# Kernel tuning notes

Hardware: AMD Instinct MI355X
Metric: run time of the kernel (lower is better)

## Reference

```python
import jax, jax.numpy as jnp
import numpy as np

B, LAT, NF, IMG, N_CALLS = 8, 512, 64, 128, 4
N_LAYERS = int(np.ceil(np.log2(IMG) - np.log2(16))) + 1  # 4 resolutions: 16,32,64,128
CF = 3  # SinSobel perception factor: identity + sobel_x + sobel_y
FIN, FH, FOUT = NF * CF, NF, NF * 2  # gated => 2*n_filter out of dyna block
P_SIZES = [FH * FIN, FH, FOUT * FH, FOUT, FOUT * FIN, FOUT]
P_OFFS = np.cumsum([0] + P_SIZES)
P_TOT = int(P_OFFS[-1])

_g1 = np.exp(-0.5 * np.array([-1.0, 0.0, 1.0]) ** 2)
_gk = np.outer(_g1, _g1); _gk = _gk / _gk.sum()
GAUSS_K = jnp.asarray(_gk, jnp.float32)
SOBEL_X = jnp.asarray(np.array([[-1, 0, 1], [-2, 0, 2], [-1, 0, 1]], np.float32) / 8.0)
SOBEL_Y = SOBEL_X.T


def _dwconv3(x, k):
    # depthwise 3x3 conv, 'same' padding; x: [B,C,H,W], k: [3,3]
    C = x.shape[1]
    kern = jnp.broadcast_to(k[None, None], (C, 1, 3, 3)).astype(x.dtype)
    return jax.lax.conv_general_dilated(
        x, kern, (1, 1), ((1, 1), (1, 1)),
        dimension_numbers=('NCHW', 'OIHW', 'NCHW'), feature_group_count=C)


def sin_sobel(x):
    # perception: [x, sobel_x(x), sobel_y(x)] -> 3*C channels
    return jnp.concatenate([x, _dwconv3(x, SOBEL_X), _dwconv3(x, SOBEL_Y)], axis=1)


def inst_norm(x, eps=1e-5):
    m = x.mean((2, 3), keepdims=True)
    v = x.var((2, 3), keepdims=True)
    return (x - m) * jax.lax.rsqrt(v + eps)


def up2_blur(x, gk):
    b, c, h, w = x.shape
    x = jax.image.resize(x, (b, c, 2 * h, 2 * w), 'bilinear')  # align_corners=False
    return _dwconv3(x, gk)


def dyna_block(x, lat, hyper_w, hyper_b):
    # hypernetwork generates per-sample 1x1-conv residual block weights
    p = lat @ hyper_w + hyper_b  # [B, P_TOT]
    w1 = p[:, P_OFFS[0]:P_OFFS[1]].reshape(-1, FH, FIN)
    b1 = p[:, P_OFFS[1]:P_OFFS[2]]
    w2 = p[:, P_OFFS[2]:P_OFFS[3]].reshape(-1, FOUT, FH)
    b2 = p[:, P_OFFS[3]:P_OFFS[4]]
    ws = p[:, P_OFFS[4]:P_OFFS[5]].reshape(-1, FOUT, FIN)
    bs = p[:, P_OFFS[5]:P_OFFS[6]]
    h = jax.nn.relu(jnp.einsum('bihw,boi->bohw', x, w1) + b1[:, :, None, None])
    y = jnp.einsum('bihw,boi->bohw', h, w2) + b2[:, :, None, None]
    s = jnp.einsum('bihw,boi->bohw', x, ws) + bs[:, :, None, None]
    return s + y


def setup_inputs() -> dict:
    key = jax.random.key(0)
    ks = jax.random.split(key, 8)
    return dict(
        lat=jax.random.normal(ks[0], (B, LAT), jnp.float32),
        ca_noise=jax.random.normal(ks[1], (B, NF, 16, 16), jnp.float32),
        seed=jax.random.normal(ks[2], (1, NF, 1, 1), jnp.float32),  # spatially constant seed
        leak_factor=jnp.asarray(0.1, jnp.float32),
        hyper_w=jax.random.normal(ks[3], (LAT, P_TOT), jnp.float32) * 0.02,
        hyper_b=jnp.zeros((P_TOT,), jnp.float32),
        res1_w=jax.random.normal(ks[4], (NF, NF), jnp.float32) / np.sqrt(NF).astype(np.float32),
        res1_b=jnp.zeros((NF,), jnp.float32),
        res2_w=jax.random.normal(ks[5], (NF, NF), jnp.float32) / np.sqrt(NF).astype(np.float32),
        res2_b=jnp.zeros((NF,), jnp.float32),
        outc_w=jax.random.normal(ks[6], (3, NF), jnp.float32) / np.sqrt(NF).astype(np.float32),
        outc_b=jnp.zeros((3,), jnp.float32),
    )


def reference(lat, ca_noise, seed, leak_factor, hyper_w, hyper_b,
              res1_w, res1_b, res2_w, res2_b, outc_w, outc_b):
    # seed init branch: constant seed -> instance_norm -> 0, plus blurred ca_noise
    out = inst_norm(jnp.broadcast_to(seed, (B, NF, 16, 16)))
    out = out + _dwconv3(ca_noise, GAUSS_K)  # in_ds (resize 16->16 is identity)
    lf = jnp.clip(leak_factor, 0.001, 1000.0)
    for c in range(N_LAYERS * N_CALLS):
        z = sin_sobel(out)
        z = inst_norm(z)
        z = dyna_block(z, lat, hyper_w, hyper_b)
        z, g = jnp.split(z, 2, axis=1)  # gated
        z = z * jax.nn.sigmoid(g)
        out = out + lf * z
        if c < N_LAYERS * N_CALLS - 1 and c % N_CALLS == N_CALLS - 1:
            out = up2_blur(out, GAUSS_K)
    # out_conv: resize to IMG is identity here; 1x1 residual block + 1x1 conv
    h = jax.nn.relu(jnp.einsum('bihw,oi->bohw', out, res1_w) + res1_b[None, :, None, None])
    r = jnp.einsum('bihw,oi->bohw', h, res2_w) + res2_b[None, :, None, None]
    y = jnp.einsum('bihw,oi->bohw', out + r, outc_w) + outc_b[None, :, None, None]
    out_raw = y
    return jnp.clip(y, -1.0, 1.0), out_raw
```

## Files before the change

### kernel.cpp

```cpp
#include <hip/hip_runtime.h>
#include <math.h>

#define B 8
#define LATD 512
#define PT 45376
#define FIN 192
#define FH 64
#define OW1 0
#define OB1 12288
#define OW2 12352
#define OB2 20544
#define OWS 20672
#define OBS 45248
#define KC 16

__device__ __forceinline__ float gk_at(int ky, int kx){
  const float a = 0.60653065971263342f;
  const float inv = 1.0f / ((1.0f + 2.0f*a) * (1.0f + 2.0f*a));
  float wy = (ky==1) ? 1.0f : a;
  float wx = (kx==1) ? 1.0f : a;
  return wy * wx * inv;
}

__global__ void k_hyper(const float* __restrict__ lat, const float* __restrict__ hw,
                        const float* __restrict__ hb, float* __restrict__ p){
  __shared__ float slat[B*LATD];
  for (int idx = threadIdx.x; idx < B*LATD; idx += 256) slat[idx] = lat[idx];
  __syncthreads();
  int j = blockIdx.x*256 + threadIdx.x;
  if (j >= PT) return;
  float acc[B];
#pragma unroll
  for (int b=0;b<B;++b) acc[b]=0.f;
  for (int k=0;k<LATD;++k){
    float w = hw[(size_t)k*PT + j];
#pragma unroll
    for (int b=0;b<B;++b) acc[b] = fmaf(slat[b*LATD+k], w, acc[b]);
  }
  float bias = hb[j];
#pragma unroll
  for (int b=0;b<B;++b) p[(size_t)b*PT + j] = acc[b] + bias;
}

__global__ void k_init(const float* __restrict__ noise, float* __restrict__ out){
  int bc = blockIdx.x;
  int t = threadIdx.x;
  int y = t >> 4, x = t & 15;
  const float* src = noise + (size_t)bc*256;
  float acc = 0.f;
#pragma unroll
  for (int ky=0;ky<3;++ky){
    int yy = y+ky-1; if (yy < 0 || yy > 15) continue;
#pragma unroll
    for (int kx=0;kx<3;++kx){
      int xx = x+kx-1; if (xx < 0 || xx > 15) continue;
      acc = fmaf(gk_at(ky,kx), src[yy*16+xx], acc);
    }
  }
  out[(size_t)bc*256 + t] = acc;
}

__global__ void __launch_bounds__(256) k_sobstat(const float* __restrict__ out, float* __restrict__ sob,
                    float* __restrict__ stats, int H, int lgH, int HW){
  int flat = blockIdx.x; int b = flat & 7, c = flat >> 3;
  int t = threadIdx.x;
  const float* src = out + ((size_t)(b*64+c))*(size_t)HW;
  float* dxp = sob + ((size_t)(b*128 + c))*(size_t)HW;
  float* dyp = sob + ((size_t)(b*128 + 64 + c))*(size_t)HW;
  float s0=0.f,q0=0.f,sx=0.f,qx=0.f,sy=0.f,qy=0.f;
  for (int px = t*4; px < HW; px += 1024){
    int y = px >> lgH, x = px & (H-1);
    float rm[6], rc[6], rp[6];
    float4 v = *(const float4*)(src + px);
    rc[1]=v.x; rc[2]=v.y; rc[3]=v.z; rc[4]=v.w;
    rc[0] = (x>0)     ? src[px-1] : 0.f;
    rc[5] = (x+4 < H) ? src[px+4] : 0.f;
    s0 += v.x+v.y+v.z+v.w;
    q0 += v.x*v.x+v.y*v.y+v.z*v.z+v.w*v.w;
    if (y > 0){
      const float* r = src + px - H;
      float4 u = *(const float4*)r;
      rm[1]=u.x; rm[2]=u.y; rm[3]=u.z; rm[4]=u.w;
      rm[0] = (x>0)     ? r[-1] : 0.f;
      rm[5] = (x+4 < H) ? r[4]  : 0.f;
    } else { rm[0]=rm[1]=rm[2]=rm[3]=rm[4]=rm[5]=0.f; }
    if (y+1 < H){
      const float* r = src + px + H;
      float4 u = *(const float4*)r;
      rp[1]=u.x; rp[2]=u.y; rp[3]=u.z; rp[4]=u.w;
      rp[0] = (x>0)     ? r[-1] : 0.f;
      rp[5] = (x+4 < H) ? r[4]  : 0.f;
    } else { rp[0]=rp[1]=rp[2]=rp[3]=rp[4]=rp[5]=0.f; }
    float dxv[4], dyv[4];
#pragma unroll
    for (int j=0;j<4;++j){
      dxv[j] = ((rm[j+2]-rm[j]) + 2.f*(rc[j+2]-rc[j]) + (rp[j+2]-rp[j])) * 0.125f;
      dyv[j] = ((rp[j] + 2.f*rp[j+1] + rp[j+2]) - (rm[j] + 2.f*rm[j+1] + rm[j+2])) * 0.125f;
      sx += dxv[j]; qx = fmaf(dxv[j],dxv[j],qx);
      sy += dyv[j]; qy = fmaf(dyv[j],dyv[j],qy);
    }
    float4 o1; o1.x=dxv[0]; o1.y=dxv[1]; o1.z=dxv[2]; o1.w=dxv[3];
    float4 o2; o2.x=dyv[0]; o2.y=dyv[1]; o2.z=dyv[2]; o2.w=dyv[3];
    *(float4*)(dxp + px) = o1;
    *(float4*)(dyp + px) = o2;
  }
  float vals[6] = {s0,q0,sx,qx,sy,qy};
  __shared__ float rbuf[6][4];
  int lane = t & 63, wid = t >> 6;
#pragma unroll
  for (int i=0;i<6;++i){
    float v = vals[i];
#pragma unroll
    for (int off=32; off; off>>=1) v += __shfl_down(v, off, 64);
    if (lane==0) rbuf[i][wid] = v;
  }
  __syncthreads();
  if (t < 3){
    float s = rbuf[t*2][0]+rbuf[t*2][1]+rbuf[t*2][2]+rbuf[t*2][3];
    float q = rbuf[t*2+1][0]+rbuf[t*2+1][1]+rbuf[t*2+1][2]+rbuf[t*2+1][3];
    float inv = 1.0f/(float)HW;
    float m = s*inv;
    float var = fmaxf(q*inv - m*m, 0.f);
    float r = 1.0f/sqrtf(var + 1e-5f);
    int ch = b*192 + c + t*64;
    stats[ch*2]   = -m*r;
    stats[ch*2+1] = r;
  }
}

__device__ __forceinline__ float4 ldx(const float* __restrict__ out, const float* __restrict__ sob,
                                      const float* __restrict__ stats,
                                      int b, int i, int off, int HW){
  const float* src = (i < 64) ? out + ((size_t)(b*64+i))*(size_t)HW
                              : sob + ((size_t)(b*128+(i-64)))*(size_t)HW;
  float4 v = *(const float4*)(src + off);
  float c = stats[(b*192+i)*2], r = stats[(b*192+i)*2+1];
  v.x = fmaf(v.x, r, c); v.y = fmaf(v.y, r, c);
  v.z = fmaf(v.z, r, c); v.w = fmaf(v.w, r, c);
  return v;
}

template<int PPT>
__global__ void __launch_bounds__(256, 3) k_dyna(float* __restrict__ out, const float* __restrict__ sob,
                       const float* __restrict__ stats, const float* __restrict__ p,
                       const float* __restrict__ lfp, int HW){
  constexpr int G     = PPT/4;
  constexpr int TPXT  = 16*PPT;
  constexpr int XST   = TPXT + 4;
  constexpr int XHALF = KC*XST;
  constexpr int W1OFF = 2*XHALF;
  constexpr int W1HALF= KC*68;
  constexpr int WEND  = W1OFF + 2*W1HALF;
  constexpr int HSZ   = 64*XST;
  constexpr int ASZ   = (WEND > HSZ) ? WEND : HSZ;
  __shared__ float bufA[ASZ];
  __shared__ float bufB[2*KC*132];

  int flat = (int)(blockIdx.y*gridDim.x + blockIdx.x);
  int b   = flat & 7;
  int px0 = (flat >> 3) * TPXT;
  int tx = threadIdx.x, ty = threadIdx.y;
  int tid = ty*16 + tx;
  const float* pw = p + (size_t)b*PT;

  float az[4][PPT], ag[4][PPT], ah[4][PPT];
#pragma unroll
  for (int k=0;k<4;++k)
#pragma unroll
    for (int j=0;j<PPT;++j){ az[k][j]=0.f; ag[k][j]=0.f; ah[k][j]=0.f; }

  const int wo0 = tid>>2, wk = tid&3, wo1 = 64 + wo0;

  float4 vx[G], vz0, vz1, v10;

  auto loadX = [&](int ci){
#pragma unroll
    for (int g=0; g<G; ++g){
      int idx = g*256 + tid;
      vx[g] = ldx(out,sob,stats,b, ci*KC + idx/(4*PPT), px0 + (idx&(4*PPT-1))*4, HW);
    }
  };
  auto loadW1z = [&](int ci){
    vz0 = *(const float4*)(pw + OWS + wo0*FIN + ci*KC + wk*4);
    vz1 = *(const float4*)(pw + OWS + wo1*FIN + ci*KC + wk*4);
    v10 = *(const float4*)(pw + OW1 + wo0*FIN + ci*KC + wk*4);
  };
  auto loadW2 = [&](int ci){
    vz0 = *(const float4*)(pw + OW2 + wo0*FH + ci*KC + wk*4);
    vz1 = *(const float4*)(pw + OW2 + wo1*FH + ci*KC + wk*4);
  };
  auto writeX = [&](int bf){
#pragma unroll
    for (int g=0; g<G; ++g){
      int idx = g*256 + tid;
      *(float4*)(&bufA[bf*XHALF + (idx/(4*PPT))*XST + (idx&(4*PPT-1))*4]) = vx[g];
    }
  };
  auto writeWz = [&](int bf){
    float* WZ = &bufB[bf*(KC*132)];
    WZ[(wk*4+0)*132+wo0]=vz0.x; WZ[(wk*4+1)*132+wo0]=vz0.y; WZ[(wk*4+2)*132+wo0]=vz0.z; WZ[(wk*4+3)*132+wo0]=vz0.w;
    WZ[(wk*4+0)*132+wo1]=vz1.x; WZ[(wk*4+1)*132+wo1]=vz1.y; WZ[(wk*4+2)*132+wo1]=vz1.z; WZ[(wk*4+3)*132+wo1]=vz1.w;
  };
  auto writeW1 = [&](int bf){
    float* W1 = &bufA[W1OFF + bf*W1HALF];
    W1[(wk*4+0)*68+wo0]=v10.x; W1[(wk*4+1)*68+wo0]=v10.y; W1[(wk*4+2)*68+wo0]=v10.z; W1[(wk*4+3)*68+wo0]=v10.w;
  };
  auto computeA = [&](int bf){
#pragma unroll 4
    for (int kk=0; kk<KC; ++kk){
      float xv[PPT];
#pragma unroll
      for (int g=0; g<G; ++g){
        float4 xa = *(const float4*)(&bufA[bf*XHALF + kk*XST + (tx+g*16)*4]);
        xv[g*4+0]=xa.x; xv[g*4+1]=xa.y; xv[g*4+2]=xa.z; xv[g*4+3]=xa.w;
      }
      float4 wz4 = *(const float4*)(&bufB[bf*(KC*132) + kk*132 + ty*4]);
      float4 wg4 = *(const float4*)(&bufB[bf*(KC*132) + kk*132 + 64 + ty*4]);
      float4 w14 = *(const float4*)(&bufA[W1OFF + bf*W1HALF + kk*68 + ty*4]);
      float wzv[4]={wz4.x,wz4.y,wz4.z,wz4.w};
      float wgv[4]={wg4.x,wg4.y,wg4.z,wg4.w};
      float w1v[4]={w14.x,w14.y,w14.z,w14.w};
#pragma unroll
      for (int k=0;k<4;++k)
#pragma unroll
        for (int j=0;j<PPT;++j){
          az[k][j] = fmaf(wzv[k], xv[j], az[k][j]);
          ag[k][j] = fmaf(wgv[k], xv[j], ag[k][j]);
          ah[k][j] = fmaf(w1v[k], xv[j], ah[k][j]);
        }
    }
  };

  loadX(0); loadW1z(0);
  writeX(0); writeWz(0); writeW1(0);
  loadX(1); loadW1z(1);
  __syncthreads();
  for (int ci=0; ci<12; ++ci){
    int cur = ci & 1;
    if (ci < 11){ writeX(cur^1); writeWz(cur^1); writeW1(cur^1); }
    if (ci < 10){ loadX(ci+2); loadW1z(ci+2); }
    else if (ci == 10){ loadW2(0); }
    computeA(cur);
    __syncthreads();
  }

#pragma unroll
  for (int k=0;k<4;++k){
    float b1 = pw[OB1 + ty*4 + k];
#pragma unroll
    for (int h=0; h<G; ++h){
      float4 r;
      r.x = fmaxf(ah[k][h*4+0]+b1, 0.f);
      r.y = fmaxf(ah[k][h*4+1]+b1, 0.f);
      r.z = fmaxf(ah[k][h*4+2]+b1, 0.f);
      r.w = fmaxf(ah[k][h*4+3]+b1, 0.f);
      *(float4*)(&bufA[(ty*4+k)*XST + (tx+h*16)*4]) = r;
    }
  }
  writeWz(0);
  loadW2(1);
  __syncthreads();

  for (int ci=0; ci<4; ++ci){
    int cur = ci & 1;
    if (ci < 3) writeWz(cur^1);
    if (ci < 2) loadW2(ci+2);
#pragma unroll 4
    for (int kk=0; kk<KC; ++kk){
      float xv[PPT];
#pragma unroll
      for (int g=0; g<G; ++g){
        float4 xa = *(const float4*)(&bufA[(ci*KC+kk)*XST + (tx+g*16)*4]);
        xv[g*4+0]=xa.x; xv[g*4+1]=xa.y; xv[g*4+2]=xa.z; xv[g*4+3]=xa.w;
      }
      float4 wz4 = *(const float4*)(&bufB[cur*(KC*132) + kk*132 + ty*4]);
      float4 wg4 = *(const float4*)(&bufB[cur*(KC*132) + kk*132 + 64 + ty*4]);
      float wzv[4]={wz4.x,wz4.y,wz4.z,wz4.w};
      float wgv[4]={wg4.x,wg4.y,wg4.z,wg4.w};
#pragma unroll
      for (int k=0;k<4;++k)
#pragma unroll
        for (int j=0;j<PPT;++j){
          az[k][j] = fmaf(wzv[k], xv[j], az[k][j]);
          ag[k][j] = fmaf(wgv[k], xv[j], ag[k][j]);
        }
    }
    __syncthreads();
  }

  float lf = fminf(fmaxf(lfp[0], 0.001f), 1000.f);
#pragma unroll
  for (int k=0;k<4;++k){
    int o = ty*4 + k;
    float bz = pw[OB2 + o]      + pw[OBS + o];
    float bg = pw[OB2 + o + 64] + pw[OBS + o + 64];
    float* op = out + ((size_t)(b*64+o))*(size_t)HW + px0;
#pragma unroll
    for (int h=0; h<G; ++h){
      float4 ov = *(const float4*)(op + (tx + h*16)*4);
      float r[4];
#pragma unroll
      for (int j=0;j<4;++j){
        float z = az[k][h*4+j] + bz;
        float g = ag[k][h*4+j] + bg;
        r[j] = lf * z / (1.f + expf(-g));
      }
      ov.x += r[0]; ov.y += r[1]; ov.z += r[2]; ov.w += r[3];
      *(float4*)(op + (tx + h*16)*4) = ov;
    }
  }
}

__global__ void k_upsample(const float* __restrict__ src, float* __restrict__ dst, int H, int lgH){
  int Hn = 2*H;
  int HWn = Hn*Hn;
  int bc = blockIdx.y;
  int o4 = (blockIdx.x*256 + threadIdx.x)*4;
  const float* s = src + (size_t)bc*(size_t)(H*H);
  int oy = o4 >> (lgH+1), ox0 = o4 & (Hn-1);
  int m = ox0 >> 1;
  int xm1 = (m-1 < 0)   ? 0   : m-1;
  int xp1 = (m+1 > H-1) ? H-1 : m+1;
  int xp2 = (m+2 > H-1) ? H-1 : m+2;
  float u[3][6];
#pragma unroll
  for (int ky=0; ky<3; ++ky){
    int yy = oy + ky - 1;
    if (yy < 0 || yy >= Hn){
#pragma unroll
      for (int j=0;j<6;++j) u[ky][j] = 0.f;
      continue;
    }
    int iy = yy >> 1, ry = yy & 1;
    int y0 = ry ? iy : iy-1;
    int y1 = ry ? iy+1 : iy;
    float wy0 = ry ? 0.75f : 0.25f;
    float wy1 = 1.f - wy0;
    y0 = y0 < 0 ? 0 : y0;
    y1 = y1 > H-1 ? H-1 : y1;
    const float* r0 = s + y0*H;
    const float* r1 = s + y1*H;
    float sv0 = wy0*r0[xm1] + wy1*r1[xm1];
    float sv1 = wy0*r0[m]   + wy1*r1[m];
    float sv2 = wy0*r0[xp1] + wy1*r1[xp1];
    float sv3 = wy0*r0[xp2] + wy1*r1[xp2];
    u[ky][0] = 0.75f*sv0 + 0.25f*sv1;
    u[ky][1] = 0.25f*sv0 + 0.75f*sv1;
    u[ky][2] = 0.75f*sv1 + 0.25f*sv2;
    u[ky][3] = 0.25f*sv1 + 0.75f*sv2;
    u[ky][4] = 0.75f*sv2 + 0.25f*sv3;
    u[ky][5] = 0.25f*sv2 + 0.75f*sv3;
    if (ox0 == 0)       u[ky][0] = 0.f;
    if (ox0 + 4 == Hn)  u[ky][5] = 0.f;
  }
  float res[4];
#pragma unroll
  for (int jo=0; jo<4; ++jo){
    float a = 0.f;
#pragma unroll
    for (int ky=0; ky<3; ++ky){
      a = fmaf(gk_at(ky,0), u[ky][jo],   a);
      a = fmaf(gk_at(ky,1), u[ky][jo+1], a);
      a = fmaf(gk_at(ky,2), u[ky][jo+2], a);
    }
    res[jo] = a;
  }
  float4 o; o.x=res[0]; o.y=res[1]; o.z=res[2]; o.w=res[3];
  *(float4*)(dst + (size_t)bc*(size_t)HWn + o4) = o;
}

__global__ void __launch_bounds__(256) k_final(const float* __restrict__ t,
    const float* __restrict__ r1w, const float* __restrict__ r1b,
    const float* __restrict__ r2w, const float* __restrict__ r2b,
    const float* __restrict__ ocw, const float* __restrict__ ocb,
    float* __restrict__ dout, int HW){
  __shared__ float Ts[64][132];
  __shared__ float Hs[64][132];
  __shared__ float Wb[64][68];
  int b = blockIdx.y;
  int tx = threadIdx.x, ty = threadIdx.y;
  int tid = ty*16 + tx;
  int px0 = blockIdx.x*128;

#pragma unroll
  for (int it=0; it<8; ++it){
    int idx = it*256 + tid;
    int ch = idx>>5, c4 = idx&31;
    *(float4*)(&Ts[ch][c4*4]) = *(const float4*)(t + ((size_t)(b*64+ch))*(size_t)HW + px0 + c4*4);
  }
#pragma unroll
  for (int it=0; it<4; ++it){
    int idx = it*256 + tid;
    int o = idx>>4, k4 = idx&15;
    float4 w = *(const float4*)(r1w + o*64 + k4*4);
    Wb[k4*4+0][o]=w.x; Wb[k4*4+1][o]=w.y; Wb[k4*4+2][o]=w.z; Wb[k4*4+3][o]=w.w;
  }
  __syncthreads();

  float acc[4][8];
#pragma unroll
  for (int k=0;k<4;++k)
#pragma unroll
    for (int j=0;j<8;++j) acc[k][j]=0.f;
#pragma unroll 4
  for (int kk=0; kk<64; ++kk){
    float4 xa = *(const float4*)(&Ts[kk][tx*4]);
    float4 xb = *(const float4*)(&Ts[kk][(tx+16)*4]);
    float4 w4 = *(const float4*)(&Wb[kk][ty*4]);
    float xv[8]={xa.x,xa.y,xa.z,xa.w,xb.x,xb.y,xb.z,xb.w};
    float wv[4]={w4.x,w4.y,w4.z,w4.w};
#pragma unroll
    for (int k=0;k<4;++k)
#pragma unroll
      for (int j=0;j<8;++j) acc[k][j] = fmaf(wv[k], xv[j], acc[k][j]);
  }
  __syncthreads();

#pragma unroll
  for (int k=0;k<4;++k){
    float bs = r1b[ty*4+k];
#pragma unroll
    for (int h=0; h<2; ++h){
      float4 r;
      r.x = fmaxf(acc[k][h*4+0]+bs, 0.f);
      r.y = fmaxf(acc[k][h*4+1]+bs, 0.f);
      r.z = fmaxf(acc[k][h*4+2]+bs, 0.f);
      r.w = fmaxf(acc[k][h*4+3]+bs, 0.f);
      *(float4*)(&Hs[ty*4+k][(tx+h*16)*4]) = r;
    }
  }
#pragma unroll
  for (int it=0; it<4; ++it){
    int idx = it*256 + tid;
    int o = idx>>4, k4 = idx&15;
    float4 w = *(const float4*)(r2w + o*64 + k4*4);
    Wb[k4*4+0][o]=w.x; Wb[k4*4+1][o]=w.y; Wb[k4*4+2][o]=w.z; Wb[k4*4+3][o]=w.w;
  }
  __syncthreads();

#pragma unroll
  for (int k=0;k<4;++k)
#pragma unroll
    for (int j=0;j<8;++j) acc[k][j]=0.f;
#pragma unroll 4
  for (int kk=0; kk<64; ++kk){
    float4 xa = *(const float4*)(&Hs[kk][tx*4]);
    float4 xb = *(const float4*)(&Hs[kk][(tx+16)*4]);
    float4 w4 = *(const float4*)(&Wb[kk][ty*4]);
    float xv[8]={xa.x,xa.y,xa.z,xa.w,xb.x,xb.y,xb.z,xb.w};
    float wv[4]={w4.x,w4.y,w4.z,w4.w};
#pragma unroll
    for (int k=0;k<4;++k)
#pragma unroll
      for (int j=0;j<8;++j) acc[k][j] = fmaf(wv[k], xv[j], acc[k][j]);
  }
#pragma unroll
  for (int k=0;k<4;++k){
    int o = ty*4 + k;
    float bs = r2b[o];
#pragma unroll
    for (int h=0; h<2; ++h){
      float4 tv = *(const float4*)(&Ts[o][(tx+h*16)*4]);
      tv.x += acc[k][h*4+0]+bs; tv.y += acc[k][h*4+1]+bs;
      tv.z += acc[k][h*4+2]+bs; tv.w += acc[k][h*4+3]+bs;
      *(float4*)(&Ts[o][(tx+h*16)*4]) = tv;
    }
  }
  __syncthreads();
  if (tid < 192){
    int c = tid>>6, kk = tid&63;
    Wb[kk][c] = ocw[c*64+kk];
  }
  __syncthreads();

  if (tid < 128){
    float a0=0.f, a1=0.f, a2=0.f;
#pragma unroll 4
    for (int kk=0; kk<64; ++kk){
      float x = Ts[kk][tid];
      a0 = fmaf(x, Wb[kk][0], a0);
      a1 = fmaf(x, Wb[kk][1], a1);
      a2 = fmaf(x, Wb[kk][2], a2);
    }
    size_t rawoff = (size_t)B*3*(size_t)HW;
    float y[3] = {a0+ocb[0], a1+ocb[1], a2+ocb[2]};
    int px = px0 + tid;
#pragma unroll
    for (int c=0;c<3;++c){
      size_t base = ((size_t)(b*3+c))*(size_t)HW + px;
      dout[base] = fminf(fmaxf(y[c],-1.f),1.f);
      dout[rawoff + base] = y[c];
    }
  }
}

extern "C" void kernel_launch(void* const* d_in, const int* in_sizes, int n_in,
                              void* d_out, int out_size, void* d_ws, size_t ws_size,
                              hipStream_t stream) {
  const float* lat = (const float*)d_in[0];
  const float* ca  = (const float*)d_in[1];
  const float* lfp = (const float*)d_in[3];
  const float* hw  = (const float*)d_in[4];
  const float* hb  = (const float*)d_in[5];
  const float* r1w = (const float*)d_in[6];
  const float* r1b = (const float*)d_in[7];
  const float* r2w = (const float*)d_in[8];
  const float* r2b = (const float*)d_in[9];
  const float* ocw = (const float*)d_in[10];
  const float* ocb = (const float*)d_in[11];
  float* dout = (float*)d_out;

  float* ws   = (float*)d_ws;
  float* p    = ws;
  float* outA = p    + (size_t)B*PT;
  float* outB = outA + (size_t)B*64*16384;
  float* sob  = outB + (size_t)B*64*16384;
  float* stats= sob  + (size_t)B*128*16384;

  k_hyper<<<dim3((PT+255)/256), dim3(256), 0, stream>>>(lat, hw, hb, p);
  k_init<<<dim3(B*64), dim3(256), 0, stream>>>(ca, outA);

  float* cur = outA;
  float* oth = outB;
  int H = 16, lgH = 4;
  for (int c = 0; c < 16; ++c){
    int HW = H*H;
    k_sobstat<<<dim3(B*64), dim3(256), 0, stream>>>(cur, sob, stats, H, lgH, HW);
    if (H >= 128)
      k_dyna<8><<<dim3(HW/128, B), dim3(16,16), 0, stream>>>(cur, sob, stats, p, lfp, HW);
    else
      k_dyna<4><<<dim3(HW/64,  B), dim3(16,16), 0, stream>>>(cur, sob, stats, p, lfp, HW);
    if (c < 15 && (c & 3) == 3){
      k_upsample<<<dim3((HW*4)/1024, B*64), dim3(256), 0, stream>>>(cur, oth, H, lgH);
      float* tmp = cur; cur = oth; oth = tmp;
      H *= 2; lgH += 1;
    }
  }
  int HW = H*H;
  k_final<<<dim3(HW/128, B), dim3(16,16), 0, stream>>>(cur, r1w, r1b, r2w, r2b, ocw, ocb, dout, HW);
}
```

Measured before the change: 1.313 ms.

## Fuse low-resolution stages into one cooperative persistent kernel with grid syncs

The first 12 CA steps (16, 32 and 64 resolution), plus the init blur and the upsamples, now run inside one cooperative kernel of 256 blocks. Grid-wide syncs separate the stages, replacing about 30 small kernel launches whose grids underfill the GPU. The sobel/stat kernel at 128 resolution now uses 1024 threads per plane instead of 256. Each grid sync has its own cost, and the persistent blocks loop over dyna tiles, so the small stages may still be latency-bound. If the cooperative launch fails, the code falls back to separate launches.

```diff
diff --git a/kernel.cpp b/kernel.cpp
--- a/kernel.cpp
+++ b/kernel.cpp
@@ -1,5 +1,8 @@
 #include <hip/hip_runtime.h>
+#include <hip/hip_cooperative_groups.h>
 #include <math.h>
+
+namespace cg = cooperative_groups;
 
 #define B 8
 #define LATD 512
@@ -60,15 +63,24 @@
   out[(size_t)bc*256 + t] = acc;
 }
 
-__global__ void __launch_bounds__(256) k_sobstat(const float* __restrict__ out, float* __restrict__ sob,
-                    float* __restrict__ stats, int H, int lgH, int HW){
-  int flat = blockIdx.x; int b = flat & 7, c = flat >> 3;
-  int t = threadIdx.x;
-  const float* src = out + ((size_t)(b*64+c))*(size_t)HW;
-  float* dxp = sob + ((size_t)(b*128 + c))*(size_t)HW;
-  float* dyp = sob + ((size_t)(b*128 + 64 + c))*(size_t)HW;
+__device__ __forceinline__ float4 ldx(const float* __restrict__ out, const float* __restrict__ sob,
+                                      const float* __restrict__ stats,
+                                      int b, int i, int off, int HW){
+  const float* src = (i < 64) ? out + ((size_t)(b*64+i))*(size_t)HW
+                              : sob + ((size_t)(b*128+(i-64)))*(size_t)HW;
+  float4 v = *(const float4*)(src + off);
+  float c = stats[(b*192+i)*2], r = stats[(b*192+i)*2+1];
+  v.x = fmaf(v.x, r, c); v.y = fmaf(v.y, r, c);
+  v.z = fmaf(v.z, r, c); v.w = fmaf(v.w, r, c);
+  return v;
+}
+
+__device__ void sobstat_body(const float* __restrict__ src, float* __restrict__ dxp,
+                             float* __restrict__ dyp, float* __restrict__ stats,
+                             float* rbufRaw, int statbase, int H, int lgH, int HW,
+                             int tid, int nthr){
   float s0=0.f,q0=0.f,sx=0.f,qx=0.f,sy=0.f,qy=0.f;
-  for (int px = t*4; px < HW; px += 1024){
+  for (int px = tid*4; px < HW; px += nthr*4){
     int y = px >> lgH, x = px & (H-1);
     float rm[6], rc[6], rp[6];
     float4 v = *(const float4*)(src + px);
@@ -105,8 +117,8 @@
     *(float4*)(dyp + px) = o2;
   }
   float vals[6] = {s0,q0,sx,qx,sy,qy};
-  __shared__ float rbuf[6][4];
-  int lane = t & 63, wid = t >> 6;
+  float (*rbuf)[16] = (float(*)[16])rbufRaw;
+  int lane = tid & 63, wid = tid >> 6;
 #pragma unroll
   for (int i=0;i<6;++i){
     float v = vals[i];
@@ -115,29 +127,291 @@
     if (lane==0) rbuf[i][wid] = v;
   }
   __syncthreads();
-  if (t < 3){
-    float s = rbuf[t*2][0]+rbuf[t*2][1]+rbuf[t*2][2]+rbuf[t*2][3];
-    float q = rbuf[t*2+1][0]+rbuf[t*2+1][1]+rbuf[t*2+1][2]+rbuf[t*2+1][3];
+  if (tid < 3){
+    int nw = nthr >> 6;
+    float s = 0.f, q = 0.f;
+    for (int i2=0;i2<nw;++i2){ s += rbuf[tid*2][i2]; q += rbuf[tid*2+1][i2]; }
     float inv = 1.0f/(float)HW;
     float m = s*inv;
     float var = fmaxf(q*inv - m*m, 0.f);
     float r = 1.0f/sqrtf(var + 1e-5f);
-    int ch = b*192 + c + t*64;
-    stats[ch*2]   = -m*r;
-    stats[ch*2+1] = r;
-  }
-}
-
-__device__ __forceinline__ float4 ldx(const float* __restrict__ out, const float* __restrict__ sob,
-                                      const float* __restrict__ stats,
-                                      int b, int i, int off, int HW){
-  const float* src = (i < 64) ? out + ((size_t)(b*64+i))*(size_t)HW
-                              : sob + ((size_t)(b*128+(i-64)))*(size_t)HW;
-  float4 v = *(const float4*)(src + off);
-  float c = stats[(b*192+i)*2], r = stats[(b*192+i)*2+1];
-  v.x = fmaf(v.x, r, c); v.y = fmaf(v.y, r, c);
-  v.z = fmaf(v.z, r, c); v.w = fmaf(v.w, r, c);
-  return v;
+    stats[(statbase + tid*64)*2]   = -m*r;
+    stats[(statbase + tid*64)*2+1] = r;
+  }
+  __syncthreads();
+}
+
+__device__ void dyna4_body(float* __restrict__ cur, const float* __restrict__ sob,
+                           const float* __restrict__ stats, const float* __restrict__ pw,
+                           float* bufA, float* bufB, int b, int px0, int HW,
+                           int tx, int ty, int tid, float lf){
+  float az[4][4], ag[4][4], ah[4][4];
+#pragma unroll
+  for (int k=0;k<4;++k)
+#pragma unroll
+    for (int j=0;j<4;++j){ az[k][j]=0.f; ag[k][j]=0.f; ah[k][j]=0.f; }
+  const int wo0 = tid>>2, wk = tid&3, wo1 = 64 + wo0;
+  float4 vx, vz0, vz1, v10;
+
+  auto loadX = [&](int ci){ vx = ldx(cur,sob,stats,b, ci*KC + ty, px0 + tx*4, HW); };
+  auto loadW1z = [&](int ci){
+    vz0 = *(const float4*)(pw + OWS + wo0*FIN + ci*KC + wk*4);
+    vz1 = *(const float4*)(pw + OWS + wo1*FIN + ci*KC + wk*4);
+    v10 = *(const float4*)(pw + OW1 + wo0*FIN + ci*KC + wk*4);
+  };
+  auto loadW2 = [&](int ci){
+    vz0 = *(const float4*)(pw + OW2 + wo0*FH + ci*KC + wk*4);
+    vz1 = *(const float4*)(pw + OW2 + wo1*FH + ci*KC + wk*4);
+  };
+  auto writeX = [&](int bf){ *(float4*)(&bufA[bf*1088 + ty*68 + tx*4]) = vx; };
+  auto writeWz = [&](int bf){
+    float* WZ = &bufB[bf*2112];
+    WZ[(wk*4+0)*132+wo0]=vz0.x; WZ[(wk*4+1)*132+wo0]=vz0.y; WZ[(wk*4+2)*132+wo0]=vz0.z; WZ[(wk*4+3)*132+wo0]=vz0.w;
+    WZ[(wk*4+0)*132+wo1]=vz1.x; WZ[(wk*4+1)*132+wo1]=vz1.y; WZ[(wk*4+2)*132+wo1]=vz1.z; WZ[(wk*4+3)*132+wo1]=vz1.w;
+  };
+  auto writeW1 = [&](int bf){
+    float* W1 = &bufA[2176 + bf*1088];
+    W1[(wk*4+0)*68+wo0]=v10.x; W1[(wk*4+1)*68+wo0]=v10.y; W1[(wk*4+2)*68+wo0]=v10.z; W1[(wk*4+3)*68+wo0]=v10.w;
+  };
+
+  loadX(0); loadW1z(0);
+  writeX(0); writeWz(0); writeW1(0);
+  loadX(1); loadW1z(1);
+  __syncthreads();
+  for (int ci=0; ci<12; ++ci){
+    int curb = ci & 1;
+    if (ci < 11){ writeX(curb^1); writeWz(curb^1); writeW1(curb^1); }
+    if (ci < 10){ loadX(ci+2); loadW1z(ci+2); }
+    else if (ci == 10){ loadW2(0); }
+#pragma unroll 4
+    for (int kk=0; kk<KC; ++kk){
+      float4 xa = *(const float4*)(&bufA[curb*1088 + kk*68 + tx*4]);
+      float4 wz4 = *(const float4*)(&bufB[curb*2112 + kk*132 + ty*4]);
+      float4 wg4 = *(const float4*)(&bufB[curb*2112 + kk*132 + 64 + ty*4]);
+      float4 w14 = *(const float4*)(&bufA[2176 + curb*1088 + kk*68 + ty*4]);
+      float xv[4]={xa.x,xa.y,xa.z,xa.w};
+      float wzv[4]={wz4.x,wz4.y,wz4.z,wz4.w};
+      float wgv[4]={wg4.x,wg4.y,wg4.z,wg4.w};
+      float w1v[4]={w14.x,w14.y,w14.z,w14.w};
+#pragma unroll
+      for (int k=0;k<4;++k)
+#pragma unroll
+        for (int j=0;j<4;++j){
+          az[k][j] = fmaf(wzv[k], xv[j], az[k][j]);
+          ag[k][j] = fmaf(wgv[k], xv[j], ag[k][j]);
+          ah[k][j] = fmaf(w1v[k], xv[j], ah[k][j]);
+        }
+    }
+    __syncthreads();
+  }
+#pragma unroll
+  for (int k=0;k<4;++k){
+    float b1 = pw[OB1 + ty*4 + k];
+    float4 r;
+    r.x = fmaxf(ah[k][0]+b1, 0.f);
+    r.y = fmaxf(ah[k][1]+b1, 0.f);
+    r.z = fmaxf(ah[k][2]+b1, 0.f);
+    r.w = fmaxf(ah[k][3]+b1, 0.f);
+    *(float4*)(&bufA[(ty*4+k)*68 + tx*4]) = r;
+  }
+  writeWz(0);
+  loadW2(1);
+  __syncthreads();
+  for (int ci=0; ci<4; ++ci){
+    int curb = ci & 1;
+    if (ci < 3) writeWz(curb^1);
+    if (ci < 2) loadW2(ci+2);
+#pragma unroll 4
+    for (int kk=0; kk<KC; ++kk){
+      float4 xa = *(const float4*)(&bufA[(ci*KC+kk)*68 + tx*4]);
+      float4 wz4 = *(const float4*)(&bufB[curb*2112 + kk*132 + ty*4]);
+      float4 wg4 = *(const float4*)(&bufB[curb*2112 + kk*132 + 64 + ty*4]);
+      float xv[4]={xa.x,xa.y,xa.z,xa.w};
+      float wzv[4]={wz4.x,wz4.y,wz4.z,wz4.w};
+      float wgv[4]={wg4.x,wg4.y,wg4.z,wg4.w};
+#pragma unroll
+      for (int k=0;k<4;++k)
+#pragma unroll
+        for (int j=0;j<4;++j){
+          az[k][j] = fmaf(wzv[k], xv[j], az[k][j]);
+          ag[k][j] = fmaf(wgv[k], xv[j], ag[k][j]);
+        }
+    }
+    __syncthreads();
+  }
+#pragma unroll
+  for (int k=0;k<4;++k){
+    int o = ty*4 + k;
+    float bz = pw[OB2 + o]      + pw[OBS + o];
+    float bg = pw[OB2 + o + 64] + pw[OBS + o + 64];
+    float* op = cur + ((size_t)(b*64+o))*(size_t)HW + px0;
+    float4 ov = *(const float4*)(op + tx*4);
+    float r[4];
+#pragma unroll
+    for (int j=0;j<4;++j){
+      float z = az[k][j] + bz;
+      float g = ag[k][j] + bg;
+      r[j] = lf * z / (1.f + expf(-g));
+    }
+    ov.x += r[0]; ov.y += r[1]; ov.z += r[2]; ov.w += r[3];
+    *(float4*)(op + tx*4) = ov;
+  }
+}
+
+__device__ void upsample_body(const float* __restrict__ s, float* __restrict__ d,
+                              int H, int lgH, int tid, int nthr){
+  int Hn = 2*H, HWn = Hn*Hn;
+  for (int o4 = tid*4; o4 < HWn; o4 += nthr*4){
+    int oy = o4 >> (lgH+1), ox0 = o4 & (Hn-1);
+    int m = ox0 >> 1;
+    int xm1 = (m-1 < 0)   ? 0   : m-1;
+    int xp1 = (m+1 > H-1) ? H-1 : m+1;
+    int xp2 = (m+2 > H-1) ? H-1 : m+2;
+    float u[3][6];
+#pragma unroll
+    for (int ky=0; ky<3; ++ky){
+      int yy = oy + ky - 1;
+      if (yy < 0 || yy >= Hn){
+#pragma unroll
+        for (int j=0;j<6;++j) u[ky][j] = 0.f;
+        continue;
+      }
+      int iy = yy >> 1, ry = yy & 1;
+      int y0 = ry ? iy : iy-1;
+      int y1 = ry ? iy+1 : iy;
+      float wy0 = ry ? 0.75f : 0.25f;
+      float wy1 = 1.f - wy0;
+      y0 = y0 < 0 ? 0 : y0;
+      y1 = y1 > H-1 ? H-1 : y1;
+      const float* r0 = s + y0*H;
+      const float* r1 = s + y1*H;
+      float sv0 = wy0*r0[xm1] + wy1*r1[xm1];
+      float sv1 = wy0*r0[m]   + wy1*r1[m];
+      float sv2 = wy0*r0[xp1] + wy1*r1[xp1];
+      float sv3 = wy0*r0[xp2] + wy1*r1[xp2];
+      u[ky][0] = 0.75f*sv0 + 0.25f*sv1;
+      u[ky][1] = 0.25f*sv0 + 0.75f*sv1;
+      u[ky][2] = 0.75f*sv1 + 0.25f*sv2;
+      u[ky][3] = 0.25f*sv1 + 0.75f*sv2;
+      u[ky][4] = 0.75f*sv2 + 0.25f*sv3;
+      u[ky][5] = 0.25f*sv2 + 0.75f*sv3;
+      if (ox0 == 0)       u[ky][0] = 0.f;
+      if (ox0 + 4 == Hn)  u[ky][5] = 0.f;
+    }
+    float res[4];
+#pragma unroll
+    for (int jo=0; jo<4; ++jo){
+      float a = 0.f;
+#pragma unroll
+      for (int ky=0; ky<3; ++ky){
+        a = fmaf(gk_at(ky,0), u[ky][jo],   a);
+        a = fmaf(gk_at(ky,1), u[ky][jo+1], a);
+        a = fmaf(gk_at(ky,2), u[ky][jo+2], a);
+      }
+      res[jo] = a;
+    }
+    float4 o; o.x=res[0]; o.y=res[1]; o.z=res[2]; o.w=res[3];
+    *(float4*)(d + o4) = o;
+  }
+}
+
+__global__ void __launch_bounds__(256, 3) k_small(float* __restrict__ outA, float* __restrict__ outB,
+    const float* __restrict__ ca, float* __restrict__ sob, float* __restrict__ stats,
+    const float* __restrict__ p, const float* __restrict__ lfp){
+  cg::grid_group grid = cg::this_grid();
+  __shared__ float bufA[4352];
+  __shared__ float bufB[4224];
+  int bid = (int)blockIdx.x;
+  int tx = threadIdx.x, ty = threadIdx.y;
+  int tid = ty*16 + tx;
+
+#pragma unroll
+  for (int it=0; it<2; ++it){
+    int bc = bid + it*256;
+    int y = tid >> 4, x = tid & 15;
+    const float* src = ca + (size_t)bc*256;
+    float acc = 0.f;
+#pragma unroll
+    for (int ky=0;ky<3;++ky){
+      int yy = y+ky-1; if (yy < 0 || yy > 15) continue;
+#pragma unroll
+      for (int kx=0;kx<3;++kx){
+        int xx = x+kx-1; if (xx < 0 || xx > 15) continue;
+        acc = fmaf(gk_at(ky,kx), src[yy*16+xx], acc);
+      }
+    }
+    outA[(size_t)bc*256 + tid] = acc;
+  }
+  grid.sync();
+
+  float* cur = outA; float* oth = outB;
+  int H = 16, lgH = 4;
+  float lf = fminf(fmaxf(lfp[0], 0.001f), 1000.f);
+
+  for (int c = 0; c < 12; ++c){
+    int HW = H*H;
+#pragma unroll
+    for (int it=0; it<2; ++it){
+      int cid = bid + it*256;
+      int b = cid & 7, ch = cid >> 3;
+      sobstat_body(cur + ((size_t)(b*64+ch))*(size_t)HW,
+                   sob + ((size_t)(b*128+ch))*(size_t)HW,
+                   sob + ((size_t)(b*128+64+ch))*(size_t)HW,
+                   stats, bufA, b*192 + ch, H, lgH, HW, tid, 256);
+    }
+    grid.sync();
+
+    int nT = (HW/64)*8;
+    for (int t = bid; t < nT; t += 256){
+      int b = t & 7;
+      int px0 = (t >> 3) * 64;
+      dyna4_body(cur, sob, stats, p + (size_t)b*PT, bufA, bufB, b, px0, HW, tx, ty, tid, lf);
+      __syncthreads();
+    }
+    grid.sync();
+
+    if ((c & 3) == 3){
+      int HWn = 4*HW;
+#pragma unroll
+      for (int it=0; it<2; ++it){
+        int plane = bid + it*256;
+        upsample_body(cur + (size_t)plane*(size_t)HW, oth + (size_t)plane*(size_t)HWn,
+                      H, lgH, tid, 256);
+      }
+      grid.sync();
+      float* tsw = cur; cur = oth; oth = tsw;
+      H *= 2; lgH += 1;
+    }
+  }
+}
+
+__global__ void __launch_bounds__(1024) k_sobstat(const float* __restrict__ out, float* __restrict__ sob,
+                    float* __restrict__ stats, int H, int lgH, int HW){
+  __shared__ float rbuf[6*16];
+  int flat = blockIdx.x; int b = flat & 7, c = flat >> 3;
+  sobstat_body(out + ((size_t)(b*64+c))*(size_t)HW,
+               sob + ((size_t)(b*128+c))*(size_t)HW,
+               sob + ((size_t)(b*128+64+c))*(size_t)HW,
+               stats, rbuf, b*192 + c, H, lgH, HW, (int)threadIdx.x, (int)blockDim.x);
+}
+
+__global__ void __launch_bounds__(256, 3) k_dyna4(float* __restrict__ out, const float* __restrict__ sob,
+                       const float* __restrict__ stats, const float* __restrict__ p,
+                       const float* __restrict__ lfp, int HW){
+  __shared__ float bufA[4352];
+  __shared__ float bufB[4224];
+  int flat = (int)(blockIdx.y*gridDim.x + blockIdx.x);
+  int b   = flat & 7;
+  int px0 = (flat >> 3) * 64;
+  float lf = fminf(fmaxf(lfp[0], 0.001f), 1000.f);
+  dyna4_body(out, sob, stats, p + (size_t)b*PT, bufA, bufB, b, px0, HW,
+             (int)threadIdx.x, (int)threadIdx.y, (int)(threadIdx.y*16+threadIdx.x), lf);
+}
+
+__global__ void k_upsample(const float* __restrict__ src, float* __restrict__ dst, int H, int lgH){
+  int bc = blockIdx.x;
+  upsample_body(src + (size_t)bc*(size_t)(H*H), dst + (size_t)bc*(size_t)(4*H*H),
+                H, lgH, (int)threadIdx.x, (int)blockDim.x);
 }
 
 template<int PPT>
@@ -170,7 +444,6 @@
     for (int j=0;j<PPT;++j){ az[k][j]=0.f; ag[k][j]=0.f; ah[k][j]=0.f; }
 
   const int wo0 = tid>>2, wk = tid&3, wo1 = 64 + wo0;
-
   float4 vx[G], vz0, vz1, v10;
 
   auto loadX = [&](int ci){
@@ -309,64 +582,6 @@
       *(float4*)(op + (tx + h*16)*4) = ov;
     }
   }
-}
-
-__global__ void k_upsample(const float* __restrict__ src, float* __restrict__ dst, int H, int lgH){
-  int Hn = 2*H;
-  int HWn = Hn*Hn;
-  int bc = blockIdx.y;
-  int o4 = (blockIdx.x*256 + threadIdx.x)*4;
-  const float* s = src + (size_t)bc*(size_t)(H*H);
-  int oy = o4 >> (lgH+1), ox0 = o4 & (Hn-1);
-  int m = ox0 >> 1;
-  int xm1 = (m-1 < 0)   ? 0   : m-1;
-  int xp1 = (m+1 > H-1) ? H-1 : m+1;
-  int xp2 = (m+2 > H-1) ? H-1 : m+2;
-  float u[3][6];
-#pragma unroll
-  for (int ky=0; ky<3; ++ky){
-    int yy = oy + ky - 1;
-    if (yy < 0 || yy >= Hn){
-#pragma unroll
-      for (int j=0;j<6;++j) u[ky][j] = 0.f;
-      continue;
-    }
-    int iy = yy >> 1, ry = yy & 1;
-    int y0 = ry ? iy : iy-1;
-    int y1 = ry ? iy+1 : iy;
-    float wy0 = ry ? 0.75f : 0.25f;
-    float wy1 = 1.f - wy0;
-    y0 = y0 < 0 ? 0 : y0;
-    y1 = y1 > H-1 ? H-1 : y1;
-    const float* r0 = s + y0*H;
-    const float* r1 = s + y1*H;
-    float sv0 = wy0*r0[xm1] + wy1*r1[xm1];
-    float sv1 = wy0*r0[m]   + wy1*r1[m];
-    float sv2 = wy0*r0[xp1] + wy1*r1[xp1];
-    float sv3 = wy0*r0[xp2] + wy1*r1[xp2];
-    u[ky][0] = 0.75f*sv0 + 0.25f*sv1;
-    u[ky][1] = 0.25f*sv0 + 0.75f*sv1;
-    u[ky][2] = 0.75f*sv1 + 0.25f*sv2;
-    u[ky][3] = 0.25f*sv1 + 0.75f*sv2;
-    u[ky][4] = 0.75f*sv2 + 0.25f*sv3;
-    u[ky][5] = 0.25f*sv2 + 0.75f*sv3;
-    if (ox0 == 0)       u[ky][0] = 0.f;
-    if (ox0 + 4 == Hn)  u[ky][5] = 0.f;
-  }
-  float res[4];
-#pragma unroll
-  for (int jo=0; jo<4; ++jo){
-    float a = 0.f;
-#pragma unroll
-    for (int ky=0; ky<3; ++ky){
-      a = fmaf(gk_at(ky,0), u[ky][jo],   a);
-      a = fmaf(gk_at(ky,1), u[ky][jo+1], a);
-      a = fmaf(gk_at(ky,2), u[ky][jo+2], a);
-    }
-    res[jo] = a;
-  }
-  float4 o; o.x=res[0]; o.y=res[1]; o.z=res[2]; o.w=res[3];
-  *(float4*)(dst + (size_t)bc*(size_t)HWn + o4) = o;
 }
 
 __global__ void __launch_bounds__(256) k_final(const float* __restrict__ t,
@@ -518,24 +733,32 @@
   float* stats= sob  + (size_t)B*128*16384;
 
   k_hyper<<<dim3((PT+255)/256), dim3(256), 0, stream>>>(lat, hw, hb, p);
-  k_init<<<dim3(B*64), dim3(256), 0, stream>>>(ca, outA);
-
-  float* cur = outA;
-  float* oth = outB;
-  int H = 16, lgH = 4;
-  for (int c = 0; c < 16; ++c){
-    int HW = H*H;
-    k_sobstat<<<dim3(B*64), dim3(256), 0, stream>>>(cur, sob, stats, H, lgH, HW);
-    if (H >= 128)
-      k_dyna<8><<<dim3(HW/128, B), dim3(16,16), 0, stream>>>(cur, sob, stats, p, lfp, HW);
-    else
-      k_dyna<4><<<dim3(HW/64,  B), dim3(16,16), 0, stream>>>(cur, sob, stats, p, lfp, HW);
-    if (c < 15 && (c & 3) == 3){
-      k_upsample<<<dim3((HW*4)/1024, B*64), dim3(256), 0, stream>>>(cur, oth, H, lgH);
-      float* tmp = cur; cur = oth; oth = tmp;
-      H *= 2; lgH += 1;
-    }
-  }
-  int HW = H*H;
+
+  void* args[] = { (void*)&outA, (void*)&outB, (void*)&ca, (void*)&sob,
+                   (void*)&stats, (void*)&p, (void*)&lfp };
+  hipError_t cerr = hipLaunchCooperativeKernel((void*)k_small, dim3(256), dim3(16,16),
+                                               args, 0, stream);
+  if (cerr != hipSuccess){
+    k_init<<<dim3(B*64), dim3(256), 0, stream>>>(ca, outA);
+    float* cur = outA; float* oth = outB;
+    int H = 16, lgH = 4;
+    for (int c = 0; c < 12; ++c){
+      int HW = H*H;
+      k_sobstat<<<dim3(B*64), dim3(256), 0, stream>>>(cur, sob, stats, H, lgH, HW);
+      k_dyna4<<<dim3(HW/64, B), dim3(16,16), 0, stream>>>(cur, sob, stats, p, lfp, HW);
+      if ((c & 3) == 3){
+        k_upsample<<<dim3(B*64), dim3(256), 0, stream>>>(cur, oth, H, lgH);
+        float* tmp = cur; cur = oth; oth = tmp;
+        H *= 2; lgH += 1;
+      }
+    }
+  }
+
+  float* cur = outB;
+  int H = 128, lgH = 7, HW = 16384;
+  for (int c = 12; c < 16; ++c){
+    k_sobstat<<<dim3(B*64), dim3(1024), 0, stream>>>(cur, sob, stats, H, lgH, HW);
+    k_dyna<8><<<dim3(HW/128, B), dim3(16,16), 0, stream>>>(cur, sob, stats, p, lfp, HW);
+  }
   k_final<<<dim3(HW/128, B), dim3(16,16), 0, stream>>>(cur, r1w, r1b, r2w, r2b, ocw, ocb, dout, HW);
 }
```

After: 2.257 ms. 1.72x slower.
